# Performance work log

Hardware: AMD Instinct MI355X
Metric: run time of the kernel (lower is better)

Reference implementation:

```python
import jax, jax.numpy as jnp
import numpy as np

D_MODEL = 1024
NHEAD = 16
HEAD_DIM = D_MODEL // NHEAD
HID = int(D_MODEL * 4.0 * (2.0 / 3.0))  # 2730, matches int(d_model*mlp_ratio*2/3)
EPS = 1e-5


def setup_inputs() -> dict:
    key = jax.random.key(0)
    ks = jax.random.split(key, 12)
    s = lambda fi, fo: (2.0 / (fi + fo)) ** 0.5
    inp = {
        "x": jax.random.normal(ks[0], (2, 2048, D_MODEL), dtype=jnp.float32),
        "ln1_w": jnp.ones((D_MODEL,), jnp.float32),
        "ln1_b": jnp.zeros((D_MODEL,), jnp.float32),
        "wq": jax.random.normal(ks[1], (D_MODEL, D_MODEL), jnp.float32) * s(D_MODEL, D_MODEL),
        "wk": jax.random.normal(ks[2], (D_MODEL, D_MODEL), jnp.float32) * s(D_MODEL, D_MODEL),
        "wv": jax.random.normal(ks[3], (D_MODEL, D_MODEL), jnp.float32) * s(D_MODEL, D_MODEL),
        "wg": jax.random.normal(ks[4], (D_MODEL, D_MODEL), jnp.float32) * s(D_MODEL, D_MODEL),
        "wo": jax.random.normal(ks[5], (D_MODEL, D_MODEL), jnp.float32) * s(D_MODEL, D_MODEL),
        "ln2_w": jnp.ones((D_MODEL,), jnp.float32),
        "ln2_b": jnp.zeros((D_MODEL,), jnp.float32),
        "w_in": jax.random.normal(ks[6], (D_MODEL, 2 * HID), jnp.float32) * s(D_MODEL, 2 * HID),
        "b_in": jnp.zeros((2 * HID,), jnp.float32),
        "w_out": jax.random.normal(ks[7], (HID, D_MODEL), jnp.float32) * s(HID, D_MODEL),
        "b_out": jnp.zeros((D_MODEL,), jnp.float32),
    }
    return inp


def _layernorm(x, w, b):
    mu = jnp.mean(x, axis=-1, keepdims=True)
    var = jnp.var(x, axis=-1, keepdims=True)
    return (x - mu) * jax.lax.rsqrt(var + EPS) * w + b


def _decay_matrix(S):
    # gamma_h = 1 - 2^{-5-h}, RetNet multiscale decays
    gamma = 1.0 - jnp.exp2(-5.0 - jnp.arange(NHEAD, dtype=jnp.float32))  # [H]
    n = jnp.arange(S, dtype=jnp.float32)
    exp = n[:, None] - n[None, :]                     # [S, S]
    mask = exp >= 0
    d = gamma[:, None, None] ** jnp.where(mask, exp, 0.0)  # [H, S, S]
    return jnp.where(mask[None], d, 0.0)


def _msr(xn, wq, wk, wv, wg, wo):
    B, S, _ = xn.shape
    split = lambda t: t.reshape(B, S, NHEAD, HEAD_DIM).transpose(0, 2, 1, 3)  # bhsd
    q = split(xn @ wq) * (HEAD_DIM ** -0.5)
    k = split(xn @ wk)
    v = split(xn @ wv)
    Dm = _decay_matrix(S)                                   # [H, S, S]
    scores = jnp.einsum("bhsd,bhtd->bhst", q, k) * Dm[None]  # causal decayed retention
    out = jnp.einsum("bhst,bhtd->bhsd", scores, v)
    # per-head normalization (GroupNorm over head dim, no affine)
    mu = jnp.mean(out, axis=-1, keepdims=True)
    var = jnp.var(out, axis=-1, keepdims=True)
    out = (out - mu) * jax.lax.rsqrt(var + 1e-6)
    out = out.transpose(0, 2, 1, 3).reshape(B, S, D_MODEL)
    out = out * jax.nn.silu(xn @ wg)                        # swish gate
    return out @ wo


def _swiglu(x, w_in, b_in, w_out, b_out):
    ab = x @ w_in + b_in
    a, b = ab[..., :HID], ab[..., HID:]
    return (a * jax.nn.silu(b)) @ w_out + b_out


def reference(x, ln1_w, ln1_b, wq, wk, wv, wg, wo, ln2_w, ln2_b, w_in, b_in, w_out, b_out):
    h = _msr(_layernorm(x, ln1_w, ln1_b), wq, wk, wv, wg, wo)
    x = x + h  # dropout/drop_path identity at eval
    x = x + _swiglu(_layernorm(x, ln2_w, ln2_b), w_in, b_in, w_out, b_out)
    return x
```

## Files before the change

kernel.cpp:

```cpp
#include <hip/hip_runtime.h>
#include <math.h>

#define D_MODEL 1024
#define NHEAD   16
#define HDIM    64
#define HID     2730
#define HID_PAD 2816
#define SEQ     2048
#define BATCH   2
#define NTOK    (BATCH * SEQ)
#define QKG     3072

typedef __attribute__((ext_vector_type(8))) short bf16x8;
typedef __attribute__((ext_vector_type(4))) float f32x4;
typedef __attribute__((ext_vector_type(4))) short s16x4;

static __device__ inline short f2bf(float f)
{
    union { float f; unsigned int u; } c; c.f = f;
    unsigned int r = c.u + 0x7FFFu + ((c.u >> 16) & 1u);
    return (short)(r >> 16);
}
static __device__ inline float bf2f(short s)
{
    union { unsigned int u; float f; } c;
    c.u = ((unsigned int)(unsigned short)s) << 16;
    return c.f;
}

#define GLD16(gsrc, ldst) \
    __builtin_amdgcn_global_load_lds((const __attribute__((address_space(1))) void*)(gsrc), \
                                     (__attribute__((address_space(3))) void*)(ldst), 16, 0, 0)


__global__ void ln_kernel(const float* __restrict__ x,
                          const float* __restrict__ w,
                          const float* __restrict__ b,
                          short* __restrict__ out,
                          float eps)
{
    int row = blockIdx.x;
    int t = threadIdx.x;
    const float4* xr = (const float4*)(x + (size_t)row * D_MODEL);
    float4 v = xr[t];
    float s  = v.x + v.y + v.z + v.w;
    float sq = v.x * v.x + v.y * v.y + v.z * v.z + v.w * v.w;
#pragma unroll
    for (int off = 32; off > 0; off >>= 1) {
        s  += __shfl_xor(s, off);
        sq += __shfl_xor(sq, off);
    }
    __shared__ float ss[4], ssq[4];
    int wave = t >> 6;
    if ((t & 63) == 0) { ss[wave] = s; ssq[wave] = sq; }
    __syncthreads();
    s  = ss[0] + ss[1] + ss[2] + ss[3];
    sq = ssq[0] + ssq[1] + ssq[2] + ssq[3];
    float mu  = s * (1.0f / D_MODEL);
    float var = sq * (1.0f / D_MODEL) - mu * mu;
    float inv = rsqrtf(var + eps);
    float4 wv = ((const float4*)w)[t];
    float4 bv = ((const float4*)b)[t];
    s16x4 o;
    o.x = f2bf((v.x - mu) * inv * wv.x + bv.x);
    o.y = f2bf((v.y - mu) * inv * wv.y + bv.y);
    o.z = f2bf((v.z - mu) * inv * wv.z + bv.z);
    o.w = f2bf((v.w - mu) * inv * wv.w + bv.w);
    *(s16x4*)(out + (size_t)row * D_MODEL + 4 * t) = o;
}

struct TJob {
    const float* src;
    short* dst;
    int ldsrc, coloff, nvalid, kvalid, KPAD, NPAD;
};
struct TJobs { TJob j[8]; };

#define TRN_BLOCKS 3392

__global__ __launch_bounds__(256) void prep_kernel(
        const float* __restrict__ x,
        const float* __restrict__ ln1w,
        const float* __restrict__ ln1b,
        short* __restrict__ xn,
        TJobs jobs)
{
    __shared__ float tile[64][65];
    __shared__ float ss[4], ssq[4];
    int bid = blockIdx.x;
    int t = threadIdx.x;

    if (bid < NTOK) {
        int row = bid;
        const float4* xr = (const float4*)(x + (size_t)row * D_MODEL);
        float4 v = xr[t];
        float s  = v.x + v.y + v.z + v.w;
        float sq = v.x * v.x + v.y * v.y + v.z * v.z + v.w * v.w;
#pragma unroll
        for (int off = 32; off > 0; off >>= 1) {
            s  += __shfl_xor(s, off);
            sq += __shfl_xor(sq, off);
        }
        int wave = t >> 6;
        if ((t & 63) == 0) { ss[wave] = s; ssq[wave] = sq; }
        __syncthreads();
        s  = ss[0] + ss[1] + ss[2] + ss[3];
        sq = ssq[0] + ssq[1] + ssq[2] + ssq[3];
        float mu  = s * (1.0f / D_MODEL);
        float var = sq * (1.0f / D_MODEL) - mu * mu;
        float inv = rsqrtf(var + 1e-5f);
        float4 wv = ((const float4*)ln1w)[t];
        float4 bv = ((const float4*)ln1b)[t];
        s16x4 o;
        o.x = f2bf((v.x - mu) * inv * wv.x + bv.x);
        o.y = f2bf((v.y - mu) * inv * wv.y + bv.y);
        o.z = f2bf((v.z - mu) * inv * wv.z + bv.z);
        o.w = f2bf((v.w - mu) * inv * wv.w + bv.w);
        *(s16x4*)(xn + (size_t)row * D_MODEL + 4 * t) = o;
        return;
    }

    int local = bid - NTOK;
    int jbi, kt, nt;
    if (local < 1280) {
        jbi = local >> 8;
        int l = local & 255;
        kt = l & 15; nt = l >> 4;
    } else if (local < 2688) {
        int l2 = local - 1280;
        jbi = 5 + (l2 >= 704 ? 1 : 0);
        int l3 = (l2 >= 704) ? l2 - 704 : l2;
        kt = l3 & 15; nt = l3 >> 4;
    } else {
        int l4 = local - 2688;
        jbi = 7;
        kt = l4 % 44; nt = l4 / 44;
    }
    TJob jb = jobs.j[jbi];
    int k0 = kt * 64, n0 = nt * 64;
    {
        int kk = t >> 2, np = (t & 3) << 4;
        int k = k0 + kk;
        bool kok = k < jb.kvalid;
        const float* srow = jb.src + (size_t)k * jb.ldsrc + jb.coloff + n0 + np;
#pragma unroll
        for (int i = 0; i < 16; ++i) {
            int n = n0 + np + i;
            tile[kk][np + i] = (kok && n < jb.nvalid) ? srow[i] : 0.0f;
        }
    }
    __syncthreads();
    {
        int nn = t >> 2, kp = (t & 3) << 4;
        short* drow = jb.dst + (size_t)(n0 + nn) * jb.KPAD + k0 + kp;
#pragma unroll
        for (int v4 = 0; v4 < 4; ++v4) {
            s16x4 o;
            o.x = f2bf(tile[kp + v4 * 4 + 0][nn]);
            o.y = f2bf(tile[kp + v4 * 4 + 1][nn]);
            o.z = f2bf(tile[kp + v4 * 4 + 2][nn]);
            o.w = f2bf(tile[kp + v4 * 4 + 3][nn]);
            *(s16x4*)(drow + v4 * 4) = o;
        }
    }
}

__global__ __launch_bounds__(256, 2) void proj_kernel(
        const short* __restrict__ xn,
        const short* __restrict__ qkgT,
        short* __restrict__ qkg,
        const short* __restrict__ wvT,
        short* __restrict__ vT)
{
    __shared__ short As[2][8192];
    __shared__ short Bs[2][4096];
    const int K = D_MODEL;
    int id = blockIdx.x;
    const short *A, *Bt;
    short* C;
    int ldc, bm, bn;
    if (id < 384) {
        A = xn; Bt = qkgT; C = qkg; ldc = QKG;
        bm = (id & 15) * 256; bn = (id >> 4) * 128;
    } else {
        int i2 = id - 384;
        A = wvT; Bt = xn; C = vT; ldc = NTOK;
        bm = (i2 & 3) * 256; bn = (i2 >> 2) * 128;
    }

    int t = threadIdx.x;
    int w = t >> 6;
    int lane = t & 63;
    int quad = lane >> 4;
    int l15  = lane & 15;
    int x7   = l15 & 7;

    int li3 = lane >> 3;
    int u   = (lane & 7) ^ li3;
    int hi  = u >> 2;
    int qk  = (u & 3) << 3;
    const short* gA = A + (size_t)(bm + hi * 128 + w * 32 + li3) * K + qk;
    const short* gB = Bt + (size_t)(bn + hi * 64 + w * 16 + li3) * K + qk;

    int abase = l15 * 64 + ((((w >> 1) << 2) | quad) ^ x7) * 8;
    int bbase = l15 * 64 + ((((w & 1) << 2) | quad) ^ x7) * 8;

    f32x4 acc[8][4];
#pragma unroll
    for (int i = 0; i < 8; ++i)
#pragma unroll
        for (int j = 0; j < 4; ++j) acc[i][j] = (f32x4){0.f, 0.f, 0.f, 0.f};

#pragma unroll
    for (int c = 0; c < 4; ++c)
        GLD16(gA + (size_t)c * 8 * K, &As[0][w * 2048 + c * 512]);
#pragma unroll
    for (int c = 0; c < 2; ++c)
        GLD16(gB + (size_t)c * 8 * K, &Bs[0][w * 1024 + c * 512]);

    for (int k0 = 0; k0 < K; k0 += 32) {
        int cur = (k0 >> 5) & 1;
        __syncthreads();
        int k1 = k0 + 32;
        if (k1 < K) {
#pragma unroll
            for (int c = 0; c < 4; ++c)
                GLD16(gA + (size_t)c * 8 * K + k1, &As[cur ^ 1][w * 2048 + c * 512]);
#pragma unroll
            for (int c = 0; c < 2; ++c)
                GLD16(gB + (size_t)c * 8 * K + k1, &Bs[cur ^ 1][w * 1024 + c * 512]);
        }
        bf16x8 af[8], bfr[4];
#pragma unroll
        for (int m = 0; m < 8; ++m)
            af[m] = *(const bf16x8*)(&As[cur][m * 1024 + abase]);
#pragma unroll
        for (int jf = 0; jf < 4; ++jf)
            bfr[jf] = *(const bf16x8*)(&Bs[cur][jf * 1024 + bbase]);
#pragma unroll
        for (int m = 0; m < 8; ++m)
#pragma unroll
            for (int jf = 0; jf < 4; ++jf)
                acc[m][jf] = __builtin_amdgcn_mfma_f32_16x16x32_bf16(af[m], bfr[jf], acc[m][jf], 0, 0, 0);
    }

#pragma unroll
    for (int m = 0; m < 8; ++m) {
        int gr = bm + (w >> 1) * 128 + m * 16 + quad * 4;
#pragma unroll
        for (int jf = 0; jf < 4; ++jf) {
            int gc = bn + (w & 1) * 64 + jf * 16 + l15;
#pragma unroll
            for (int r = 0; r < 4; ++r)
                C[(size_t)(gr + r) * ldc + gc] = f2bf(acc[m][jf][r]);
        }
    }
}

template<int EPI>
__global__ __launch_bounds__(256, 4) void gemm_n64(
        const short* __restrict__ A, int lda,
        const short* __restrict__ Bt,
        const float* __restrict__ bias,
        const float* __restrict__ R, int ldr,
        void* __restrict__ C, int ldc, int K)
{
    __shared__ short As[2][4096];
    __shared__ short Bs[2][2048];
    int bm = blockIdx.x * 128;
    int bn = blockIdx.y * 64;
    int t = threadIdx.x;
    int w = t >> 6;
    int lane = t & 63;
    int quad = lane >> 4;
    int l15  = lane & 15;
    int x7   = l15 & 7;

    int p0 = t >> 3;
    int u  = (t & 7) ^ (p0 & 7);
    int scol = (u & 3) << 3;
    const short* gA0 = A  + (size_t)(bm + p0 + ((u >> 2) << 6)) * lda + scol;
    const short* gA1 = gA0 + (size_t)32 * lda;
    const short* gB0 = Bt + (size_t)(bn + p0 + ((u >> 2) << 5)) * K + scol;
    int wb = w << 9;

    int wr = (w >> 1) * 64;
    int wc = (w & 1) * 32;
    int aoff = l15 * 64 + (((((w >> 1) << 2) | quad) ^ x7) << 3);
    int boff = l15 * 64 + (((((w & 1) << 2) | quad) ^ x7) << 3);

    f32x4 acc[4][2];
#pragma unroll
    for (int i = 0; i < 4; ++i)
#pragma unroll
        for (int j = 0; j < 2; ++j) acc[i][j] = (f32x4){0.f, 0.f, 0.f, 0.f};

    GLD16(gA0, &As[0][wb]);
    GLD16(gA1, &As[0][2048 + wb]);
    GLD16(gB0, &Bs[0][wb]);

    for (int k0 = 0; k0 < K; k0 += 32) {
        int cur = (k0 >> 5) & 1;
        __syncthreads();
        int k1 = k0 + 32;
        if (k1 < K) {
            GLD16(gA0 + k1, &As[cur ^ 1][wb]);
            GLD16(gA1 + k1, &As[cur ^ 1][2048 + wb]);
            GLD16(gB0 + k1, &Bs[cur ^ 1][wb]);
        }
        bf16x8 af[4], bfr[2];
#pragma unroll
        for (int i = 0; i < 4; ++i)
            af[i] = *(const bf16x8*)(&As[cur][i * 1024 + aoff]);
#pragma unroll
        for (int j = 0; j < 2; ++j)
            bfr[j] = *(const bf16x8*)(&Bs[cur][j * 1024 + boff]);
#pragma unroll
        for (int i = 0; i < 4; ++i)
#pragma unroll
            for (int j = 0; j < 2; ++j)
                acc[i][j] = __builtin_amdgcn_mfma_f32_16x16x32_bf16(af[i], bfr[j], acc[i][j], 0, 0, 0);
    }

#pragma unroll
    for (int i = 0; i < 4; ++i) {
        int gr = bm + wr + i * 16 + quad * 4;
#pragma unroll
        for (int j = 0; j < 2; ++j) {
            int gc = bn + wc + j * 16 + l15;
#pragma unroll
            for (int r = 0; r < 4; ++r) {
                float val = acc[i][j][r];
                size_t idx = (size_t)(gr + r) * ldc + gc;
                if (EPI == 0) {
                    ((short*)C)[idx] = f2bf(val);
                } else if (EPI == 1) {
                    ((float*)C)[idx] = val + R[(size_t)(gr + r) * ldr + gc];
                } else {
                    ((float*)C)[idx] = val + bias[gc] + R[(size_t)(gr + r) * ldr + gc];
                }
            }
        }
    }
}

__global__ __launch_bounds__(256, 2) void mlp_fused(
        const short* __restrict__ A,
        const short* __restrict__ w_inT,
        const float* __restrict__ b_in,
        short* __restrict__ hm)
{
    __shared__ short As[2][8192];
    __shared__ short Bs[2][4096];
    const int K = D_MODEL;
    int bm = blockIdx.x * 256;
    int bn = blockIdx.y * 64;
    int t = threadIdx.x;
    int w = t >> 6;
    int lane = t & 63;
    int quad = lane >> 4;
    int l15  = lane & 15;
    int x7   = l15 & 7;

    int li3 = lane >> 3;
    int u   = (lane & 7) ^ li3;
    int hi  = u >> 2;
    int qk  = (u & 3) << 3;
    const short* gA = A + (size_t)(bm + hi * 128 + w * 32 + li3) * K + qk;
    int f = hi * 4 + w;
    const short* gB = w_inT + (size_t)(((f & 1) ? HID_PAD : 0) + bn
                                       + ((f >> 1) << 4) + li3) * K + qk;

    int abase = l15 * 64 + ((((w >> 1) << 2) | quad) ^ x7) * 8;
    int bbase = l15 * 64 + ((((w & 1) << 2) | quad) ^ x7) * 8;

    f32x4 acc[8][4];
#pragma unroll
    for (int i = 0; i < 8; ++i)
#pragma unroll
        for (int j = 0; j < 4; ++j) acc[i][j] = (f32x4){0.f, 0.f, 0.f, 0.f};

#pragma unroll
    for (int c = 0; c < 4; ++c)
        GLD16(gA + (size_t)c * 8 * K, &As[0][w * 2048 + c * 512]);
#pragma unroll
    for (int c = 0; c < 2; ++c)
        GLD16(gB + (size_t)c * 8 * K, &Bs[0][w * 1024 + c * 512]);

    for (int k0 = 0; k0 < K; k0 += 32) {
        int cur = (k0 >> 5) & 1;
        __syncthreads();
        int k1 = k0 + 32;
        if (k1 < K) {
#pragma unroll
            for (int c = 0; c < 4; ++c)
                GLD16(gA + (size_t)c * 8 * K + k1, &As[cur ^ 1][w * 2048 + c * 512]);
#pragma unroll
            for (int c = 0; c < 2; ++c)
                GLD16(gB + (size_t)c * 8 * K + k1, &Bs[cur ^ 1][w * 1024 + c * 512]);
        }
        bf16x8 af[8], bfr[4];
#pragma unroll
        for (int m = 0; m < 8; ++m)
            af[m] = *(const bf16x8*)(&As[cur][m * 1024 + abase]);
#pragma unroll
        for (int jf = 0; jf < 4; ++jf)
            bfr[jf] = *(const bf16x8*)(&Bs[cur][jf * 1024 + bbase]);
#pragma unroll
        for (int m = 0; m < 8; ++m)
#pragma unroll
            for (int jf = 0; jf < 4; ++jf)
                acc[m][jf] = __builtin_amdgcn_mfma_f32_16x16x32_bf16(af[m], bfr[jf], acc[m][jf], 0, 0, 0);
    }

#pragma unroll
    for (int m = 0; m < 8; ++m) {
        int gr = bm + (w >> 1) * 128 + m * 16 + quad * 4;
#pragma unroll
        for (int jj = 0; jj < 2; ++jj) {
            int gc = bn + (((w & 1) << 1) + jj) * 16 + l15;
            bool ok = gc < HID;
            float ba = ok ? b_in[gc] : 0.0f;
            float bb = ok ? b_in[HID + gc] : 0.0f;
#pragma unroll
            for (int r = 0; r < 4; ++r) {
                float a  = acc[m][2 * jj][r] + ba;
                float bv = acc[m][2 * jj + 1][r] + bb;
                float val = ok ? a * (bv / (1.0f + expf(-bv))) : 0.0f;
                hm[(size_t)(gr + r) * HID_PAD + gc] = f2bf(val);
            }
        }
    }
}

#define PSTR 72

__global__ __launch_bounds__(512) void retention_mfma(
        const short* __restrict__ qkg,
        const short* __restrict__ vT,
        short* __restrict__ rg)
{
    int i  = blockIdx.x;
    int xg = i & 15;
    int h  = (i >> 4) & 15;
    int b  = i >> 8;
    int qb = b ? xg : 15 - xg;

    __shared__ short ks[2][4096];
    __shared__ short vt[2][4096];
    __shared__ short ps[8][16 * PSTR];

    int tid  = threadIdx.x;
    int w    = tid >> 6;
    int lane = tid & 63;
    int quad = lane >> 4;
    int l15  = lane & 15;
    int x7   = l15 & 7;

    float log2g = log1pf(-exp2f(-5.0f - (float)h)) * 1.4426950408889634f;
    int hcol = h * HDIM;
    int s0 = qb * 128;
    size_t tok0 = (size_t)b * SEQ;

    int sch  = tid >> 8;
    int p0r  = (tid >> 3) & 31;
    int ur   = (tid & 7) ^ (p0r & 7);
    int srw  = p0r + ((ur >> 2) << 5);
    int sc8  = (ur & 3) << 3;
    const short* kbase  = qkg + (tok0 + srw) * QKG + 1024 + hcol + sch * 32 + sc8;
    const short* vtbase = vT + (size_t)(hcol + srw) * NTOK + tok0 + sch * 32 + sc8;
    int lb = tid << 3;

    const short* qrow = qkg + (tok0 + s0 + w * 16 + l15) * QKG + hcol;
    bf16x8 qa0 = *(const bf16x8*)(qrow + quad * 8);
    bf16x8 qa1 = *(const bf16x8*)(qrow + 32 + quad * 8);

    float colfac[4];
#pragma unroll
    for (int tile = 0; tile < 4; ++tile)
        colfac[tile] = exp2f(-(float)(tile * 16 + l15) * log2g) * 0.125f;

    f32x4 oacc[4];
#pragma unroll
    for (int k = 0; k < 4; ++k) oacc[k] = (f32x4){0.f, 0.f, 0.f, 0.f};

    int sbase = s0 + w * 16 + quad * 4;
    int tmax = 2 * qb + 1;

    float rf[4];
#pragma unroll
    for (int reg = 0; reg < 4; ++reg)
        rf[reg] = exp2f((float)(sbase + reg) * log2g);
    float gstep = exp2f(-64.0f * log2g);

    GLD16(kbase, &ks[0][lb]);
    GLD16(vtbase, &vt[0][lb]);

    for (int tb = 0; tb <= tmax; ++tb) {
        int cur = tb & 1;
        __syncthreads();
        if (tb < tmax) {
            GLD16(kbase + (size_t)(tb + 1) * 64 * QKG, &ks[cur ^ 1][lb]);
            GLD16(vtbase + (tb + 1) * 64, &vt[cur ^ 1][lb]);
        }

        f32x4 sacc[4];
#pragma unroll
        for (int k = 0; k < 4; ++k) sacc[k] = (f32x4){0.f, 0.f, 0.f, 0.f};
#pragma unroll
        for (int tile = 0; tile < 4; ++tile) {
            int kaddr = ((tile & 1) * 16 + l15) * 64 +
                        (((((tile >> 1) << 2) | quad) ^ x7) << 3);
            bf16x8 kb0 = *(const bf16x8*)(&ks[cur][kaddr]);
            bf16x8 kb1 = *(const bf16x8*)(&ks[cur][2048 + kaddr]);
            sacc[tile] = __builtin_amdgcn_mfma_f32_16x16x32_bf16(qa0, kb0, sacc[tile], 0, 0, 0);
            sacc[tile] = __builtin_amdgcn_mfma_f32_16x16x32_bf16(qa1, kb1, sacc[tile], 0, 0, 0);
        }

        int fbi = sbase - tb * 64;

        if (tb * 64 + 63 > s0 + w * 16) {
#pragma unroll
            for (int tile = 0; tile < 4; ++tile) {
                int tt = tile * 16 + l15;
#pragma unroll
                for (int reg = 0; reg < 4; ++reg) {
                    float p = (fbi + reg >= tt) ? sacc[tile][reg] * rf[reg] * colfac[tile] : 0.0f;
                    ps[w][(quad * 4 + reg) * PSTR + tile * 16 + l15] = f2bf(p);
                }
            }
        } else {
#pragma unroll
            for (int tile = 0; tile < 4; ++tile)
#pragma unroll
                for (int reg = 0; reg < 4; ++reg)
                    ps[w][(quad * 4 + reg) * PSTR + tile * 16 + l15] =
                        f2bf(sacc[tile][reg] * (rf[reg] * colfac[tile]));
        }
#pragma unroll
        for (int reg = 0; reg < 4; ++reg)
            rf[reg] *= gstep;

#pragma unroll
        for (int ksi = 0; ksi < 2; ++ksi) {
            bf16x8 pa = *(const bf16x8*)(&ps[w][l15 * PSTR + ksi * 32 + quad * 8]);
#pragma unroll
            for (int dt = 0; dt < 4; ++dt) {
                int vaddr = ((dt & 1) * 16 + l15) * 64 +
                            (((((dt >> 1) << 2) | quad) ^ x7) << 3);
                bf16x8 vb = *(const bf16x8*)(&vt[cur][ksi * 2048 + vaddr]);
                oacc[dt] = __builtin_amdgcn_mfma_f32_16x16x32_bf16(pa, vb, oacc[dt], 0, 0, 0);
            }
        }
    }

    float s1[4], s2[4];
#pragma unroll
    for (int reg = 0; reg < 4; ++reg) {
        s1[reg] = oacc[0][reg] + oacc[1][reg] + oacc[2][reg] + oacc[3][reg];
        s2[reg] = oacc[0][reg] * oacc[0][reg] + oacc[1][reg] * oacc[1][reg]
                + oacc[2][reg] * oacc[2][reg] + oacc[3][reg] * oacc[3][reg];
    }
#pragma unroll
    for (int off = 1; off < 16; off <<= 1) {
#pragma unroll
        for (int reg = 0; reg < 4; ++reg) {
            s1[reg] += __shfl_xor(s1[reg], off);
            s2[reg] += __shfl_xor(s2[reg], off);
        }
    }
    size_t rowtok = tok0 + s0 + w * 16 + quad * 4;
    short* obase = rg + rowtok * D_MODEL + hcol;
    const short* gbase = qkg + rowtok * QKG + 2048 + hcol;
#pragma unroll
    for (int reg = 0; reg < 4; ++reg) {
        float mu  = s1[reg] * (1.0f / 64.0f);
        float var = s2[reg] * (1.0f / 64.0f) - mu * mu;
        float inv = rsqrtf(var + 1e-6f);
#pragma unroll
        for (int dt = 0; dt < 4; ++dt) {
            float gv = bf2f(gbase[(size_t)reg * QKG + dt * 16 + l15]);
            float val = (oacc[dt][reg] - mu) * inv * (gv / (1.0f + expf(-gv)));
            obase[(size_t)reg * D_MODEL + dt * 16 + l15] = f2bf(val);
        }
    }
}

extern "C" void kernel_launch(void* const* d_in, const int* in_sizes, int n_in,
                              void* d_out, int out_size, void* d_ws, size_t ws_size,
                              hipStream_t stream)
{
    const float* x     = (const float*)d_in[0];
    const float* ln1w  = (const float*)d_in[1];
    const float* ln1b  = (const float*)d_in[2];
    const float* wq    = (const float*)d_in[3];
    const float* wk    = (const float*)d_in[4];
    const float* wv    = (const float*)d_in[5];
    const float* wg    = (const float*)d_in[6];
    const float* wo    = (const float*)d_in[7];
    const float* ln2w  = (const float*)d_in[8];
    const float* ln2b  = (const float*)d_in[9];
    const float* w_in  = (const float*)d_in[10];
    const float* b_in  = (const float*)d_in[11];
    const float* w_out = (const float*)d_in[12];
    const float* b_out = (const float*)d_in[13];
    float* out = (float*)d_out;
    char* base = (char*)d_ws;

    const size_t MB = 1u << 20;
    short* xn     = (short*)(base);
    short* qkgT   = (short*)(base +  8 * MB);
    short* wvT    = (short*)(base + 14 * MB);
    short* woT    = (short*)(base + 16 * MB);
    short* w_inT  = (short*)(base + 18 * MB);
    short* w_outT = (short*)(base + 29 * MB);
    short* qkg    = (short*)(base + 35 * MB);
    short* hm     = (short*)(base + 35 * MB);
    short* vT     = (short*)(base + 59 * MB);
    short* rg     = (short*)(base + 67 * MB);

    TJobs jobs;
    jobs.j[0] = { wq,    qkgT,                          1024,    0, 1024, 1024, 1024, 1024 };
    jobs.j[1] = { wk,    qkgT + 1024 * 1024,            1024,    0, 1024, 1024, 1024, 1024 };
    jobs.j[2] = { wg,    qkgT + 2 * 1024 * 1024,        1024,    0, 1024, 1024, 1024, 1024 };
    jobs.j[3] = { wv,    wvT,                           1024,    0, 1024, 1024, 1024, 1024 };
    jobs.j[4] = { wo,    woT,                           1024,    0, 1024, 1024, 1024, 1024 };
    jobs.j[5] = { w_in,  w_inT,                         2 * HID, 0,   HID, 1024, 1024, HID_PAD };
    jobs.j[6] = { w_in,  w_inT + (size_t)HID_PAD * 1024, 2 * HID, HID, HID, 1024, 1024, HID_PAD };
    jobs.j[7] = { w_out, w_outT,                        1024,    0, 1024, HID, HID_PAD, 1024 };

    prep_kernel<<<NTOK + TRN_BLOCKS, 256, 0, stream>>>(x, ln1w, ln1b, xn, jobs);
    proj_kernel<<<512, 256, 0, stream>>>(xn, qkgT, qkg, wvT, vT);
    retention_mfma<<<512, 512, 0, stream>>>(qkg, vT, rg);
    gemm_n64<1><<<dim3(32, 16), 256, 0, stream>>>(rg, D_MODEL, woT, nullptr, x, D_MODEL, out, D_MODEL, D_MODEL);
    ln_kernel<<<NTOK, 256, 0, stream>>>(out, ln2w, ln2b, xn, 1e-5f);
    mlp_fused<<<dim3(NTOK / 256, HID_PAD / 64), 256, 0, stream>>>(xn, w_inT, b_in, hm);
    gemm_n64<2><<<dim3(32, 16), 256, 0, stream>>>(hm, HID_PAD, w_outT, b_out, out, D_MODEL, out, D_MODEL, HID_PAD);
}
```

Baseline: 375.3 us.

## Split retention blocks to 64-row query tiles with 4 waves, halving P scratch

The retention kernel now launches 1024 blocks of 256 threads, each covering 64 query rows instead of 128, with the grid index reordered so the head varies fastest. Each thread loads two 16-byte chunks per K/V tile, and the decayed score tile is written to shared memory in 32-column halves that are consumed immediately by the PV MFMA. This reduces per-block shared memory and should improve occupancy and load balance across the causal triangle. In exchange, K/V tiles are re-fetched by twice as many blocks, which adds global and L2 traffic.

```diff
diff --git a/kernel.cpp b/kernel.cpp
--- a/kernel.cpp
+++ b/kernel.cpp
@@ -433,22 +433,23 @@
     }
 }
 
-#define PSTR 72
-
-__global__ __launch_bounds__(512) void retention_mfma(
+#define PSH 36
+
+__global__ __launch_bounds__(256) void retention_mfma(
         const short* __restrict__ qkg,
         const short* __restrict__ vT,
         short* __restrict__ rg)
 {
     int i  = blockIdx.x;
-    int xg = i & 15;
-    int h  = (i >> 4) & 15;
-    int b  = i >> 8;
-    int qb = b ? xg : 15 - xg;
+    int h  = i & 15;
+    int t5 = i >> 4;
+    int b  = t5 >> 5;
+    int m  = t5 & 31;
+    int j  = b ? m : 31 - m;
 
     __shared__ short ks[2][4096];
     __shared__ short vt[2][4096];
-    __shared__ short ps[8][16 * PSTR];
+    __shared__ short ps[4][16 * PSH];
 
     int tid  = threadIdx.x;
     int w    = tid >> 6;
@@ -459,16 +460,16 @@
 
     float log2g = log1pf(-exp2f(-5.0f - (float)h)) * 1.4426950408889634f;
     int hcol = h * HDIM;
-    int s0 = qb * 128;
+    int s0 = j * 64;
     size_t tok0 = (size_t)b * SEQ;
 
-    int sch  = tid >> 8;
-    int p0r  = (tid >> 3) & 31;
-    int ur   = (tid & 7) ^ (p0r & 7);
-    int srw  = p0r + ((ur >> 2) << 5);
-    int sc8  = (ur & 3) << 3;
-    const short* kbase  = qkg + (tok0 + srw) * QKG + 1024 + hcol + sch * 32 + sc8;
-    const short* vtbase = vT + (size_t)(hcol + srw) * NTOK + tok0 + sch * 32 + sc8;
+    int p0 = tid >> 3;
+    int g  = tid & 7;
+    int ur = g ^ (p0 & 7);
+    int srw = p0 + ((ur >> 2) << 5);
+    int sc8 = (ur & 3) << 3;
+    const short* kbase = qkg + (tok0 + srw) * QKG + 1024 + hcol + sc8;
+    const short* vbase = vT + (size_t)(hcol + srw) * NTOK + tok0 + sc8;
     int lb = tid << 3;
 
     const short* qrow = qkg + (tok0 + s0 + w * 16 + l15) * QKG + hcol;
@@ -485,7 +486,7 @@
     for (int k = 0; k < 4; ++k) oacc[k] = (f32x4){0.f, 0.f, 0.f, 0.f};
 
     int sbase = s0 + w * 16 + quad * 4;
-    int tmax = 2 * qb + 1;
+    int tmax = j;
 
     float rf[4];
 #pragma unroll
@@ -493,15 +494,21 @@
         rf[reg] = exp2f((float)(sbase + reg) * log2g);
     float gstep = exp2f(-64.0f * log2g);
 
-    GLD16(kbase, &ks[0][lb]);
-    GLD16(vtbase, &vt[0][lb]);
+    GLD16(kbase,      &ks[0][lb]);
+    GLD16(kbase + 32, &ks[0][2048 + lb]);
+    GLD16(vbase,      &vt[0][lb]);
+    GLD16(vbase + 32, &vt[0][2048 + lb]);
 
     for (int tb = 0; tb <= tmax; ++tb) {
         int cur = tb & 1;
         __syncthreads();
         if (tb < tmax) {
-            GLD16(kbase + (size_t)(tb + 1) * 64 * QKG, &ks[cur ^ 1][lb]);
-            GLD16(vtbase + (tb + 1) * 64, &vt[cur ^ 1][lb]);
+            size_t ko = (size_t)(tb + 1) * 64 * QKG;
+            int    vo = (tb + 1) * 64;
+            GLD16(kbase + ko,      &ks[cur ^ 1][lb]);
+            GLD16(kbase + ko + 32, &ks[cur ^ 1][2048 + lb]);
+            GLD16(vbase + vo,      &vt[cur ^ 1][lb]);
+            GLD16(vbase + vo + 32, &vt[cur ^ 1][2048 + lb]);
         }
 
         f32x4 sacc[4];
@@ -518,32 +525,32 @@
         }
 
         int fbi = sbase - tb * 64;
-
-        if (tb * 64 + 63 > s0 + w * 16) {
-#pragma unroll
-            for (int tile = 0; tile < 4; ++tile) {
-                int tt = tile * 16 + l15;
-#pragma unroll
-                for (int reg = 0; reg < 4; ++reg) {
-                    float p = (fbi + reg >= tt) ? sacc[tile][reg] * rf[reg] * colfac[tile] : 0.0f;
-                    ps[w][(quad * 4 + reg) * PSTR + tile * 16 + l15] = f2bf(p);
+        bool needmask = (tb * 64 + 63 > s0 + w * 16);
+
+#pragma unroll
+        for (int ksi = 0; ksi < 2; ++ksi) {
+            if (needmask) {
+#pragma unroll
+                for (int th = 0; th < 2; ++th) {
+                    int tile = ksi * 2 + th;
+                    int tt = tile * 16 + l15;
+#pragma unroll
+                    for (int reg = 0; reg < 4; ++reg) {
+                        float p = (fbi + reg >= tt) ? sacc[tile][reg] * rf[reg] * colfac[tile] : 0.0f;
+                        ps[w][(quad * 4 + reg) * PSH + th * 16 + l15] = f2bf(p);
+                    }
+                }
+            } else {
+#pragma unroll
+                for (int th = 0; th < 2; ++th) {
+                    int tile = ksi * 2 + th;
+#pragma unroll
+                    for (int reg = 0; reg < 4; ++reg)
+                        ps[w][(quad * 4 + reg) * PSH + th * 16 + l15] =
+                            f2bf(sacc[tile][reg] * (rf[reg] * colfac[tile]));
                 }
             }
-        } else {
-#pragma unroll
-            for (int tile = 0; tile < 4; ++tile)
-#pragma unroll
-                for (int reg = 0; reg < 4; ++reg)
-                    ps[w][(quad * 4 + reg) * PSTR + tile * 16 + l15] =
-                        f2bf(sacc[tile][reg] * (rf[reg] * colfac[tile]));
-        }
-#pragma unroll
-        for (int reg = 0; reg < 4; ++reg)
-            rf[reg] *= gstep;
-
-#pragma unroll
-        for (int ksi = 0; ksi < 2; ++ksi) {
-            bf16x8 pa = *(const bf16x8*)(&ps[w][l15 * PSTR + ksi * 32 + quad * 8]);
+            bf16x8 pa = *(const bf16x8*)(&ps[w][l15 * PSH + quad * 8]);
 #pragma unroll
             for (int dt = 0; dt < 4; ++dt) {
                 int vaddr = ((dt & 1) * 16 + l15) * 64 +
@@ -552,6 +559,9 @@
                 oacc[dt] = __builtin_amdgcn_mfma_f32_16x16x32_bf16(pa, vb, oacc[dt], 0, 0, 0);
             }
         }
+#pragma unroll
+        for (int reg = 0; reg < 4; ++reg)
+            rf[reg] *= gstep;
     }
 
     float s1[4], s2[4];
@@ -631,7 +641,7 @@
 
     prep_kernel<<<NTOK + TRN_BLOCKS, 256, 0, stream>>>(x, ln1w, ln1b, xn, jobs);
     proj_kernel<<<512, 256, 0, stream>>>(xn, qkgT, qkg, wvT, vT);
-    retention_mfma<<<512, 512, 0, stream>>>(qkg, vT, rg);
+    retention_mfma<<<1024, 256, 0, stream>>>(qkg, vT, rg);
     gemm_n64<1><<<dim3(32, 16), 256, 0, stream>>>(rg, D_MODEL, woT, nullptr, x, D_MODEL, out, D_MODEL, D_MODEL);
     ln_kernel<<<NTOK, 256, 0, stream>>>(out, ln2w, ln2b, xn, 1e-5f);
     mlp_fused<<<dim3(NTOK / 256, HID_PAD / 64), 256, 0, stream>>>(xn, w_inT, b_in, hm);
```

Measured after the change: 377.1 us. No clear change (+0.5%).
